# Performance work log

Hardware: AMD Instinct MI355X
Metric: run time of the kernel (lower is better)

## Reference

```python
import jax, jax.numpy as jnp
import numpy as np
from jax import lax

B, S, F_IN, H = 64, 512, 128, 512

def setup_inputs() -> dict:
    key = jax.random.key(0)
    ks = jax.random.split(key, 7)
    s = 1.0 / np.sqrt(H)
    return {
        "inputs": jax.random.normal(ks[0], (B, S, F_IN), dtype=jnp.float32),
        "W_ih": jax.random.normal(ks[1], (4 * H, F_IN), dtype=jnp.float32) * s,
        "W_hh": jax.random.normal(ks[2], (4 * H, H), dtype=jnp.float32) * s,
        "b_ih": jax.random.normal(ks[3], (4 * H,), dtype=jnp.float32) * s,
        "b_hh": jax.random.normal(ks[4], (4 * H,), dtype=jnp.float32) * s,
        "W_out": jax.random.normal(ks[5], (F_IN, H), dtype=jnp.float32) * s,
        "b_out": jax.random.normal(ks[6], (F_IN,), dtype=jnp.float32) * s,
    }

def reference(inputs, W_ih, W_hh, b_ih, b_hh, W_out, b_out):
    # inputs: [B, S, F]. Inference path: y=None, future=0 -> scan over all S steps.
    b, seq, _ = inputs.shape
    h = W_hh.shape[1]
    # Precompute input-to-gate projections for all timesteps: [S, B, 4H]
    x_gates = jnp.einsum("bsf,gf->sbg", inputs, W_ih) + b_ih + b_hh

    def step(carry, xg):
        h_t, c_t = carry
        gates = xg + h_t @ W_hh.T  # [B, 4H]
        i_g, f_g, g_g, o_g = jnp.split(gates, 4, axis=-1)
        i_g = jax.nn.sigmoid(i_g)
        f_g = jax.nn.sigmoid(f_g)
        g_g = jnp.tanh(g_g)
        o_g = jax.nn.sigmoid(o_g)
        c_t = f_g * c_t + i_g * g_g
        h_t = o_g * jnp.tanh(c_t)
        out = h_t @ W_out.T + b_out  # [B, F]
        return (h_t, c_t), out

    h0 = jnp.zeros((b, h), dtype=inputs.dtype)
    c0 = jnp.zeros((b, h), dtype=inputs.dtype)
    _, outs = lax.scan(step, (h0, c0), x_gates)  # outs: [S, B, F]
    return jnp.transpose(outs, (1, 0, 2))  # [B, S, F]
```

## Files before the change

kernel.cpp:

```cpp
#include <hip/hip_runtime.h>

typedef float f32x4 __attribute__((ext_vector_type(4)));

namespace {
constexpr int Bn = 64, Sn = 512, Fn = 128, Hn = 512;
constexpr int NWG = 512, NTHR = 512;
constexpr int HXS = 644;
constexpr int PQS = 293;
constexpr int RING0 = 1024;
constexpr int GRP_RING = 8192;
}

__device__ __forceinline__ float sigmoid_f(float v) {
    return 1.0f / (1.0f + __expf(-v));
}
__device__ __forceinline__ float tanh_f(float v) {
    v = fminf(fmaxf(v, -15.0f), 15.0f);
    const float e = __expf(-2.0f * v);
    return (1.0f - e) / (1.0f + e);
}

__global__ __launch_bounds__(NTHR)
__attribute__((amdgpu_waves_per_eu(4, 4)))
void lstm_persist(const float* __restrict__ x,
                  const float* __restrict__ Wih,
                  const float* __restrict__ Whh,
                  const float* __restrict__ bih,
                  const float* __restrict__ bhh,
                  const float* __restrict__ Wout,
                  const float* __restrict__ bout,
                  float* __restrict__ out,
                  float* __restrict__ ws)
{
    const int t = threadIdx.x;

    __shared__ int s_grp[2];
    if (t == 0) {
        const unsigned xcc =
            (unsigned)__builtin_amdgcn_s_getreg(20 | (0 << 6) | (3 << 11)) & 7u;
        unsigned* slotp = (unsigned*)ws + 256 + 32 * xcc;
        s_grp[0] = (int)xcc;
        s_grp[1] = (int)(atomicAdd(slotp, 1u) & 63u);
    }
    __syncthreads();
    const int bw = s_grp[0];
    const int rw = s_grp[1];

    unsigned* const gcnt = (unsigned*)ws + 32 * bw;
    float* const ring = ws + RING0 + (size_t)bw * GRP_RING;

    const int q  = t & 31;
    const int r2 = t >> 5;
    const int k0 = 20 * q;

    const int out_fi  = t & 1;
    const int out_bb  = (t >> 1) & 7;
    const int out_ksl = t >> 4;

    __shared__ float hx[8][HXS];
    __shared__ float part[32 * PQS];
    __shared__ float opart[2][8][17];
    __shared__ float gb[32];
    __shared__ float cst[8][9];
    __shared__ float bo[2];

    f32x4 wreg[2][5];
#pragma unroll
    for (int i = 0; i < 2; ++i) {
        const int r = 2 * r2 + i;
        const int G = (r >> 3) * Hn + rw * 8 + (r & 7);
#pragma unroll
        for (int j = 0; j < 5; ++j) {
            const int kk = k0 + 4 * j;
            if (kk < Hn) wreg[i][j] = *(const f32x4*)(Whh + (size_t)G * Hn + kk);
            else         wreg[i][j] = *(const f32x4*)(Wih + (size_t)G * Fn + (kk - Hn));
        }
    }

    if (t < 32) {
        const int G = (t >> 3) * Hn + rw * 8 + (t & 7);
        gb[t] = bih[G] + bhh[G];
    }
    if (t < 2) bo[t] = bout[rw * 2 + t];
    if (t < 64) cst[t >> 3][t & 7] = 0.0f;

    if (t < 64) {
        const int ul = t & 7, bbc = t >> 3;
        float* hdst = ring + 4096 + (size_t)bbc * 512 + (8 * rw + ul);
        const float z = 0.0f;
        asm volatile("global_store_dword %0, %1, off sc0"
                     :: "v"(hdst), "v"(z) : "memory");
    }
    asm volatile("s_waitcnt vmcnt(0)" ::: "memory");
    __syncthreads();
    if (t == 0) {
        atomicAdd(gcnt, 1u);
        int guard = 0;
        while (__hip_atomic_load(gcnt, __ATOMIC_RELAXED,
                                 __HIP_MEMORY_SCOPE_AGENT) < 64u) {
            __builtin_amdgcn_s_sleep(1);
            if (++guard > 1000000) break;
        }
    }
    __syncthreads();

    for (int k = 0; k <= Sn; ++k) {
        const int slot = (k & 1) ^ 1;
        {
            const float* p0 = ring + (size_t)slot * 4096 + 4 * t;
            const float* p1 = p0 + 2048;
            f32x4 v0, v1;
            asm volatile(
                "global_load_dwordx4 %0, %2, off sc0\n\t"
                "global_load_dwordx4 %1, %3, off sc0\n\t"
                "s_waitcnt vmcnt(0)"
                : "=&v"(v0), "=&v"(v1)
                : "v"(p0), "v"(p1) : "memory");
            int fi = t;
            *(f32x4*)&hx[fi >> 7][(fi & 127) * 4] = v0;
            fi = t + 512;
            *(f32x4*)&hx[fi >> 7][(fi & 127) * 4] = v1;
        }
        if (k < Sn && t < 256) {
            const int bbs = t >> 5, f4 = (t & 31) * 4;
            const f32x4 v = *(const f32x4*)(x + (size_t)(8 * bw + bbs) * Sn * Fn +
                                            (size_t)k * Fn + f4);
            *(f32x4*)&hx[bbs][Hn + f4] = v;
        }
        __syncthreads();

        if (k < Sn) {
            float acc[2][8];
#pragma unroll
            for (int i = 0; i < 2; ++i)
#pragma unroll
                for (int ib = 0; ib < 8; ++ib) acc[i][ib] = 0.0f;
#pragma unroll
            for (int j = 0; j < 5; ++j) {
                f32x4 hv[4];
#pragma unroll
                for (int ib = 0; ib < 4; ++ib)
                    hv[ib] = *(const f32x4*)&hx[ib][k0 + 4 * j];
#pragma unroll
                for (int i = 0; i < 2; ++i)
#pragma unroll
                    for (int ib = 0; ib < 4; ++ib)
                        acc[i][ib] += wreg[i][j].x * hv[ib].x + wreg[i][j].y * hv[ib].y +
                                      wreg[i][j].z * hv[ib].z + wreg[i][j].w * hv[ib].w;
#pragma unroll
                for (int ib = 0; ib < 4; ++ib)
                    hv[ib] = *(const f32x4*)&hx[4 + ib][k0 + 4 * j];
#pragma unroll
                for (int i = 0; i < 2; ++i)
#pragma unroll
                    for (int ib = 0; ib < 4; ++ib)
                        acc[i][4 + ib] += wreg[i][j].x * hv[ib].x + wreg[i][j].y * hv[ib].y +
                                          wreg[i][j].z * hv[ib].z + wreg[i][j].w * hv[ib].w;
            }
#pragma unroll
            for (int i = 0; i < 2; ++i)
#pragma unroll
                for (int ib = 0; ib < 8; ++ib)
                    part[q * PQS + (2 * r2 + i) * 9 + ib] = acc[i][ib];
        }

        if (k >= 1 && t < 256) {
            const float* wo = Wout + (size_t)(rw * 2 + out_fi) * Hn + out_ksl * 32;
            const float* hrow = &hx[out_bb][out_ksl * 32];
            float oa = 0.0f;
#pragma unroll
            for (int jj = 0; jj < 8; ++jj) {
                const f32x4 wv = *(const f32x4*)(wo + 4 * jj);
                const f32x4 hv = *(const f32x4*)(hrow + 4 * jj);
                oa += wv.x * hv.x + wv.y * hv.y + wv.z * hv.z + wv.w * hv.w;
            }
            opart[out_fi][out_bb][out_ksl] = oa;
        }
        __syncthreads();

        if (k < Sn && t < 128) {
            const int gh = t & 1, ul = (t >> 1) & 7, bbc = (t >> 4) & 7;
            const int r0 = 16 * gh + ul, r1 = 16 * gh + 8 + ul;
            float s0 = gb[r0], s1 = gb[r1];
#pragma unroll
            for (int qq = 0; qq < 32; ++qq) {
                s0 += part[qq * PQS + r0 * 9 + bbc];
                s1 += part[qq * PQS + r1 * 9 + bbc];
            }
            const float o0 = __shfl_xor(s0, 1, 64);
            const float o1 = __shfl_xor(s1, 1, 64);
            if (gh == 0) {
                const float ig = sigmoid_f(s0);
                const float fg = sigmoid_f(s1);
                const float gg = tanh_f(o0);
                const float og = sigmoid_f(o1);
                const float cn = fg * cst[ul][bbc] + ig * gg;
                cst[ul][bbc] = cn;
                const float hn = og * tanh_f(cn);
                float* hdst = ring + (size_t)(k & 1) * 4096 +
                              (size_t)bbc * 512 + (8 * rw + ul);
                asm volatile("global_store_dword %0, %1, off sc0"
                             :: "v"(hdst), "v"(hn) : "memory");
            }
        } else if (k >= 1 && t >= 256 && t < 272) {
            const int fi = (t - 256) >> 3, bbo = (t - 256) & 7;
            float s = bo[fi];
#pragma unroll
            for (int qq = 0; qq < 16; ++qq) s += opart[fi][bbo][qq];
            out[(size_t)(8 * bw + bbo) * Sn * Fn + (size_t)(k - 1) * Fn +
                rw * 2 + fi] = s;
        }

        if (k < Sn) {
            asm volatile("s_waitcnt vmcnt(0)" ::: "memory");
            __syncthreads();
            if (t == 0) {
                atomicAdd(gcnt, 1u);
                const unsigned target = 64u * (unsigned)(k + 2);
                int guard = 0;
                while (__hip_atomic_load(gcnt, __ATOMIC_RELAXED,
                                         __HIP_MEMORY_SCOPE_AGENT) < target) {
                    __builtin_amdgcn_s_sleep(1);
                    if (++guard > 100000) break;
                }
            }
            __syncthreads();
        }
    }
}

extern "C" void kernel_launch(void* const* d_in, const int* in_sizes, int n_in,
                              void* d_out, int out_size, void* d_ws, size_t ws_size,
                              hipStream_t stream) {
    (void)in_sizes; (void)n_in; (void)out_size; (void)ws_size;
    const float* x    = (const float*)d_in[0];
    const float* Wih  = (const float*)d_in[1];
    const float* Whh  = (const float*)d_in[2];
    const float* bih  = (const float*)d_in[3];
    const float* bhh  = (const float*)d_in[4];
    const float* Wout = (const float*)d_in[5];
    const float* bout = (const float*)d_in[6];
    float* outp = (float*)d_out;
    float* wsp  = (float*)d_ws;

    hipMemsetAsync(d_ws, 0, 4096, stream);

    lstm_persist<<<dim3(NWG), dim3(NTHR), 0, stream>>>(
        x, Wih, Whh, bih, bhh, Wout, bout, outp, wsp);
}
```

Measured before the change: 8.306 ms.

## Double persistent workgroups to halve per-workgroup hidden units and gate rows

Launches 1024 persistent workgroups instead of 512, so each owns 4 hidden units (16 gate rows) and one output feature instead of 8 units and two features. Each thread now holds one weight row slice in registers, and the partial-sum, output-reduction and cell-state buffers shrink to match. Occupancy is raised to 8 waves per EU. The aim is to cut per-step compute latency on the serial recurrence critical path. In exchange each group barrier now waits on 128 arrivals per XCC instead of 64, and the h-broadcast reads are duplicated across twice as many workgroups.

```diff
diff --git a/kernel.cpp b/kernel.cpp
--- a/kernel.cpp
+++ b/kernel.cpp
@@ -4,9 +4,9 @@
 
 namespace {
 constexpr int Bn = 64, Sn = 512, Fn = 128, Hn = 512;
-constexpr int NWG = 512, NTHR = 512;
+constexpr int NWG = 1024, NTHR = 512;
 constexpr int HXS = 644;
-constexpr int PQS = 293;
+constexpr int PQS = 145;
 constexpr int RING0 = 1024;
 constexpr int GRP_RING = 8192;
 }
@@ -21,7 +21,7 @@
 }
 
 __global__ __launch_bounds__(NTHR)
-__attribute__((amdgpu_waves_per_eu(4, 4)))
+__attribute__((amdgpu_waves_per_eu(8, 8)))
 void lstm_persist(const float* __restrict__ x,
                   const float* __restrict__ Wih,
                   const float* __restrict__ Whh,
@@ -40,7 +40,7 @@
             (unsigned)__builtin_amdgcn_s_getreg(20 | (0 << 6) | (3 << 11)) & 7u;
         unsigned* slotp = (unsigned*)ws + 256 + 32 * xcc;
         s_grp[0] = (int)xcc;
-        s_grp[1] = (int)(atomicAdd(slotp, 1u) & 63u);
+        s_grp[1] = (int)(atomicAdd(slotp, 1u) & 127u);
     }
     __syncthreads();
     const int bw = s_grp[0];
@@ -49,44 +49,41 @@
     unsigned* const gcnt = (unsigned*)ws + 32 * bw;
     float* const ring = ws + RING0 + (size_t)bw * GRP_RING;
 
-    const int q  = t & 31;
-    const int r2 = t >> 5;
+    const int q = t & 31;
+    const int r = t >> 5;
     const int k0 = 20 * q;
 
-    const int out_fi  = t & 1;
-    const int out_bb  = (t >> 1) & 7;
-    const int out_ksl = t >> 4;
+    const int out_bb  = t & 7;
+    const int out_ksl = (t >> 3) & 31;
 
     __shared__ float hx[8][HXS];
     __shared__ float part[32 * PQS];
-    __shared__ float opart[2][8][17];
-    __shared__ float gb[32];
-    __shared__ float cst[8][9];
-    __shared__ float bo[2];
-
-    f32x4 wreg[2][5];
-#pragma unroll
-    for (int i = 0; i < 2; ++i) {
-        const int r = 2 * r2 + i;
-        const int G = (r >> 3) * Hn + rw * 8 + (r & 7);
+    __shared__ float opart[8][33];
+    __shared__ float gb[16];
+    __shared__ float cst[4][9];
+    __shared__ float bo[1];
+
+    f32x4 wreg[5];
+    {
+        const int G = (r >> 2) * Hn + rw * 4 + (r & 3);
 #pragma unroll
         for (int j = 0; j < 5; ++j) {
             const int kk = k0 + 4 * j;
-            if (kk < Hn) wreg[i][j] = *(const f32x4*)(Whh + (size_t)G * Hn + kk);
-            else         wreg[i][j] = *(const f32x4*)(Wih + (size_t)G * Fn + (kk - Hn));
-        }
-    }
+            if (kk < Hn) wreg[j] = *(const f32x4*)(Whh + (size_t)G * Hn + kk);
+            else         wreg[j] = *(const f32x4*)(Wih + (size_t)G * Fn + (kk - Hn));
+        }
+    }
+
+    if (t < 16) {
+        const int G = (t >> 2) * Hn + rw * 4 + (t & 3);
+        gb[t] = bih[G] + bhh[G];
+    }
+    if (t == 0) bo[0] = bout[rw];
+    if (t < 32) cst[t >> 3][t & 7] = 0.0f;
 
     if (t < 32) {
-        const int G = (t >> 3) * Hn + rw * 8 + (t & 7);
-        gb[t] = bih[G] + bhh[G];
-    }
-    if (t < 2) bo[t] = bout[rw * 2 + t];
-    if (t < 64) cst[t >> 3][t & 7] = 0.0f;
-
-    if (t < 64) {
-        const int ul = t & 7, bbc = t >> 3;
-        float* hdst = ring + 4096 + (size_t)bbc * 512 + (8 * rw + ul);
+        const int ul = t & 3, bbc = t >> 2;
+        float* hdst = ring + 4096 + (size_t)bbc * 512 + (4 * rw + ul);
         const float z = 0.0f;
         asm volatile("global_store_dword %0, %1, off sc0"
                      :: "v"(hdst), "v"(z) : "memory");
@@ -97,7 +94,7 @@
         atomicAdd(gcnt, 1u);
         int guard = 0;
         while (__hip_atomic_load(gcnt, __ATOMIC_RELAXED,
-                                 __HIP_MEMORY_SCOPE_AGENT) < 64u) {
+                                 __HIP_MEMORY_SCOPE_AGENT) < 128u) {
             __builtin_amdgcn_s_sleep(1);
             if (++guard > 1000000) break;
         }
@@ -130,11 +127,9 @@
         __syncthreads();
 
         if (k < Sn) {
-            float acc[2][8];
-#pragma unroll
-            for (int i = 0; i < 2; ++i)
-#pragma unroll
-                for (int ib = 0; ib < 8; ++ib) acc[i][ib] = 0.0f;
+            float acc[8];
+#pragma unroll
+            for (int ib = 0; ib < 8; ++ib) acc[ib] = 0.0f;
 #pragma unroll
             for (int j = 0; j < 5; ++j) {
                 f32x4 hv[4];
@@ -142,45 +137,39 @@
                 for (int ib = 0; ib < 4; ++ib)
                     hv[ib] = *(const f32x4*)&hx[ib][k0 + 4 * j];
 #pragma unroll
-                for (int i = 0; i < 2; ++i)
-#pragma unroll
-                    for (int ib = 0; ib < 4; ++ib)
-                        acc[i][ib] += wreg[i][j].x * hv[ib].x + wreg[i][j].y * hv[ib].y +
-                                      wreg[i][j].z * hv[ib].z + wreg[i][j].w * hv[ib].w;
+                for (int ib = 0; ib < 4; ++ib)
+                    acc[ib] += wreg[j].x * hv[ib].x + wreg[j].y * hv[ib].y +
+                               wreg[j].z * hv[ib].z + wreg[j].w * hv[ib].w;
 #pragma unroll
                 for (int ib = 0; ib < 4; ++ib)
                     hv[ib] = *(const f32x4*)&hx[4 + ib][k0 + 4 * j];
 #pragma unroll
-                for (int i = 0; i < 2; ++i)
-#pragma unroll
-                    for (int ib = 0; ib < 4; ++ib)
-                        acc[i][4 + ib] += wreg[i][j].x * hv[ib].x + wreg[i][j].y * hv[ib].y +
-                                          wreg[i][j].z * hv[ib].z + wreg[i][j].w * hv[ib].w;
-            }
-#pragma unroll
-            for (int i = 0; i < 2; ++i)
-#pragma unroll
-                for (int ib = 0; ib < 8; ++ib)
-                    part[q * PQS + (2 * r2 + i) * 9 + ib] = acc[i][ib];
+                for (int ib = 0; ib < 4; ++ib)
+                    acc[4 + ib] += wreg[j].x * hv[ib].x + wreg[j].y * hv[ib].y +
+                                   wreg[j].z * hv[ib].z + wreg[j].w * hv[ib].w;
+            }
+#pragma unroll
+            for (int ib = 0; ib < 8; ++ib)
+                part[q * PQS + r * 9 + ib] = acc[ib];
         }
 
         if (k >= 1 && t < 256) {
-            const float* wo = Wout + (size_t)(rw * 2 + out_fi) * Hn + out_ksl * 32;
-            const float* hrow = &hx[out_bb][out_ksl * 32];
+            const float* wo = Wout + (size_t)rw * Hn + out_ksl * 16;
+            const float* hrow = &hx[out_bb][out_ksl * 16];
             float oa = 0.0f;
 #pragma unroll
-            for (int jj = 0; jj < 8; ++jj) {
+            for (int jj = 0; jj < 4; ++jj) {
                 const f32x4 wv = *(const f32x4*)(wo + 4 * jj);
                 const f32x4 hv = *(const f32x4*)(hrow + 4 * jj);
                 oa += wv.x * hv.x + wv.y * hv.y + wv.z * hv.z + wv.w * hv.w;
             }
-            opart[out_fi][out_bb][out_ksl] = oa;
+            opart[out_bb][out_ksl] = oa;
         }
         __syncthreads();
 
-        if (k < Sn && t < 128) {
-            const int gh = t & 1, ul = (t >> 1) & 7, bbc = (t >> 4) & 7;
-            const int r0 = 16 * gh + ul, r1 = 16 * gh + 8 + ul;
+        if (k < Sn && t < 64) {
+            const int gh = t & 1, ul = (t >> 1) & 3, bbc = (t >> 3) & 7;
+            const int r0 = 8 * gh + ul, r1 = 8 * gh + 4 + ul;
             float s0 = gb[r0], s1 = gb[r1];
 #pragma unroll
             for (int qq = 0; qq < 32; ++qq) {
@@ -198,17 +187,16 @@
                 cst[ul][bbc] = cn;
                 const float hn = og * tanh_f(cn);
                 float* hdst = ring + (size_t)(k & 1) * 4096 +
-                              (size_t)bbc * 512 + (8 * rw + ul);
+                              (size_t)bbc * 512 + (4 * rw + ul);
                 asm volatile("global_store_dword %0, %1, off sc0"
                              :: "v"(hdst), "v"(hn) : "memory");
             }
-        } else if (k >= 1 && t >= 256 && t < 272) {
-            const int fi = (t - 256) >> 3, bbo = (t - 256) & 7;
-            float s = bo[fi];
-#pragma unroll
-            for (int qq = 0; qq < 16; ++qq) s += opart[fi][bbo][qq];
-            out[(size_t)(8 * bw + bbo) * Sn * Fn + (size_t)(k - 1) * Fn +
-                rw * 2 + fi] = s;
+        } else if (k >= 1 && t >= 256 && t < 264) {
+            const int bbo = t - 256;
+            float s = bo[0];
+#pragma unroll
+            for (int qq = 0; qq < 32; ++qq) s += opart[bbo][qq];
+            out[(size_t)(8 * bw + bbo) * Sn * Fn + (size_t)(k - 1) * Fn + rw] = s;
         }
 
         if (k < Sn) {
@@ -216,7 +204,7 @@
             __syncthreads();
             if (t == 0) {
                 atomicAdd(gcnt, 1u);
-                const unsigned target = 64u * (unsigned)(k + 2);
+                const unsigned target = 128u * (unsigned)(k + 2);
                 int guard = 0;
                 while (__hip_atomic_load(gcnt, __ATOMIC_RELAXED,
                                          __HIP_MEMORY_SCOPE_AGENT) < target) {
```

After: 8.323 ms. About the same (+0.2%).
